# Kernel optimization log

Hardware: AMD Instinct MI355X
Metric: run time of the kernel (lower is better)

Reference implementation:

```python
import jax, jax.numpy as jnp
import numpy as np

D_MODEL = 1024
NUM_HEADS = 16
D_K = D_MODEL // NUM_HEADS
ROPE_THETA = 10000.0


def apply_rope(x, pos):
    # x: [B, H, S, d_k], pos: [S] int
    half = x.shape[-1] // 2
    inv_freq = ROPE_THETA ** (-jnp.arange(half, dtype=jnp.float32) * 2.0 / x.shape[-1])
    ang = pos.astype(jnp.float32)[:, None] * inv_freq[None, :]  # [S, half]
    cos, sin = jnp.cos(ang), jnp.sin(ang)
    x1 = x[..., 0::2]
    x2 = x[..., 1::2]
    r1 = x1 * cos - x2 * sin
    r2 = x1 * sin + x2 * cos
    return jnp.stack([r1, r2], axis=-1).reshape(x.shape)


def setup_inputs() -> dict:
    key = jax.random.key(0)
    ks = jax.random.split(key, 5)
    B, S = 4, 2048
    scale = 1.0 / np.sqrt(D_MODEL)
    x = jax.random.normal(ks[0], (B, S, D_MODEL), dtype=jnp.float32)
    w_q = jax.random.normal(ks[1], (D_MODEL, D_MODEL), dtype=jnp.float32) * scale
    w_k = jax.random.normal(ks[2], (D_MODEL, D_MODEL), dtype=jnp.float32) * scale
    w_v = jax.random.normal(ks[3], (D_MODEL, D_MODEL), dtype=jnp.float32) * scale
    w_o = jax.random.normal(ks[4], (D_MODEL, D_MODEL), dtype=jnp.float32) * scale
    token_positions = jnp.arange(S, dtype=jnp.int32)
    return {"x": x, "w_q": w_q, "w_k": w_k, "w_v": w_v, "w_o": w_o, "token_positions": token_positions}


def reference(x, w_q, w_k, w_v, w_o, token_positions):
    B, S, _ = x.shape
    def proj(w):
        return (x @ w.T).reshape(B, S, NUM_HEADS, D_K).transpose(0, 2, 1, 3)  # [B,H,S,d_k]
    q, k, v = proj(w_q), proj(w_k), proj(w_v)
    q = apply_rope(q, token_positions)
    k = apply_rope(k, token_positions)
    logits = jnp.einsum('bhid,bhjd->bhij', q, k) / jnp.sqrt(jnp.float32(D_K))
    causal = jnp.tril(jnp.ones((S, S), dtype=bool))
    logits = jnp.where(causal[None, None], logits, -jnp.inf)
    weights = jax.nn.softmax(logits, axis=-1)
    attn = jnp.einsum('bhij,bhjd->bhid', weights, v)  # [B,H,S,d_k]
    attn = attn.transpose(0, 2, 1, 3).reshape(B, S, D_MODEL)
    return attn @ w_o.T
```

## Files before the change

### kernel.cpp

```cpp
#include <hip/hip_runtime.h>
#include <hip/hip_bf16.h>
#include <stdint.h>

#define DM   1024
#define SEQ  2048
#define BATCH 4
#define NH   16
#define DK   64
#define NTK  16

typedef __attribute__((ext_vector_type(8))) __bf16 bf16x8;
typedef __attribute__((ext_vector_type(4))) float f32x4;
typedef __attribute__((ext_vector_type(4))) unsigned short ushort4_t;

typedef __attribute__((address_space(1))) const unsigned int GU32;
typedef __attribute__((address_space(3))) unsigned int LU32;

__device__ inline void gl_lds16(const void* g, void* l) {
  __builtin_amdgcn_global_load_lds((GU32*)g, (LU32*)l, 16, 0, 0);
}

__device__ inline f32x4 mfma16(bf16x8 a, bf16x8 b, f32x4 c) {
  return __builtin_amdgcn_mfma_f32_16x16x32_bf16(a, b, c, 0, 0, 0);
}

__device__ inline unsigned short f2bf(float f) {
  unsigned u = __float_as_uint(f);
  u += 0x7fffu + ((u >> 16) & 1u);
  return (unsigned short)(u >> 16);
}

__device__ inline unsigned cvt_pk_bf16(float a, float b) {
  unsigned r;
  asm("v_cvt_pk_bf16_f32 %0, %1, %2" : "=v"(r) : "v"(a), "v"(b));
  return r;
}

__device__ inline float fexp2(float x) {
  float r;
  asm("v_exp_f32 %0, %1" : "=v"(r) : "v"(x));
  return r;
}

__device__ inline int swz_of(int r) { return ((r & 6) << 2) | ((r & 1) << 5); }
__device__ inline int bswz(int r) { return ((r & 6) << 3) | ((r & 1) << 6); }

__global__ void prep_kernel(const float* __restrict__ x,
                            const float* __restrict__ wq, const float* __restrict__ wk,
                            const float* __restrict__ wv, const float* __restrict__ wo,
                            const int* __restrict__ tp,
                            unsigned short* __restrict__ xbf,
                            unsigned short* __restrict__ wbf,
                            float2* __restrict__ tab)
{
  const int NX4 = (BATCH*SEQ*DM)/4;
  const int NW4 = (DM*DM)/4;
  int idx = blockIdx.x*256 + threadIdx.x;
  if (idx < NX4) {
    float4 v = ((const float4*)x)[idx];
    ushort4_t o; o[0]=f2bf(v.x); o[1]=f2bf(v.y); o[2]=f2bf(v.z); o[3]=f2bf(v.w);
    ((ushort4_t*)xbf)[idx] = o;
  } else if (idx < NX4 + 4*NW4) {
    int t = idx - NX4;
    int wsel = t >> 18;
    int off = t & (NW4-1);
    const float* src = (wsel==0) ? wq : (wsel==1) ? wk : (wsel==2) ? wv : wo;
    float4 v = ((const float4*)src)[off];
    ushort4_t o; o[0]=f2bf(v.x); o[1]=f2bf(v.y); o[2]=f2bf(v.z); o[3]=f2bf(v.w);
    ((ushort4_t*)wbf)[wsel*NW4 + off] = o;
  } else {
    int t = idx - NX4 - 4*NW4;
    if (t < SEQ*32) {
      int s = t >> 5, i = t & 31;
      float invf = exp2f(-(float)i * (13.287712379549449f/32.0f));
      float ang = (float)tp[s] * invf;
      float sn, cs; sincosf(ang, &sn, &cs);
      tab[t] = make_float2(cs, sn);
    }
  }
}

template<int MODE>
__global__ __launch_bounds__(256, 2)
void gemm_db(const unsigned short* __restrict__ A,
             const unsigned short* __restrict__ Wall,
             unsigned short* __restrict__ qbf,
             unsigned short* __restrict__ kbf,
             unsigned short* __restrict__ vt,
             float* __restrict__ ofp,
             const float2* __restrict__ tab)
{
  __shared__ __align__(16) char lds[65536];
  const int tid = threadIdx.x;
  const int bid = blockIdx.x;
  int sel, mt, nt;
  if (MODE == 0) {
    sel = bid >> 9;
    int r = bid & 511;
    int xcd = r & 7, idx = r >> 3;
    mt = xcd*8 + (idx >> 3);  nt = idx & 7;
  } else {
    sel = 3;
    int xcd = bid & 7, idx = bid >> 3;
    mt = xcd*8 + (idx >> 3);  nt = idx & 7;
  }
  const unsigned short* Bm = Wall + (size_t)sel*DM*DM;
  const int a0 = mt*128, b0r = nt*128;
  const int w = tid>>6, lane = tid&63, ln = lane&15, g = lane>>4;
  const int wm = (w>>1)*64, wn = (w&1)*64;

  const char* src[8];
  {
    int rr = tid >> 3;
    int c  = (tid & 7) * 8;
    #pragma unroll
    for (int i = 0; i < 4; ++i) {
      int r_ = i*32 + rr;
      int cs = c ^ swz_of(r_);
      src[i]   = (const char*)(A  + (size_t)(a0  + r_)*DM + cs);
      src[i+4] = (const char*)(Bm + (size_t)(b0r + r_)*DM + cs);
    }
  }

  int offA[4], offB[4];
  #pragma unroll
  for (int m = 0; m < 4; ++m) {
    int R  = wm + m*16 + ln;
    offA[m] = R*128 + ((g*8 ^ swz_of(R)) * 2);
    int Rb = wn + m*16 + ln;
    offB[m] = 16384 + Rb*128 + ((g*8 ^ swz_of(Rb)) * 2);
  }

  f32x4 acc[4][4];
  #pragma unroll
  for (int i=0;i<4;i++)
    #pragma unroll
    for (int j=0;j<4;j++) acc[i][j] = (f32x4){0.f,0.f,0.f,0.f};

  #pragma unroll
  for (int i = 0; i < 8; ++i) gl_lds16(src[i],       lds +         i*4096 + tid*16);
  #pragma unroll
  for (int i = 0; i < 8; ++i) gl_lds16(src[i] + 128, lds + 32768 + i*4096 + tid*16);

  for (int t = 0; t < NTK; ++t) {
    char* sb = lds + (t & 1) * 32768;
    if (t < NTK-1) asm volatile("s_waitcnt vmcnt(8)" ::: "memory");
    else           asm volatile("s_waitcnt vmcnt(0)" ::: "memory");
    __builtin_amdgcn_sched_barrier(0);
    __builtin_amdgcn_s_barrier();
    asm volatile("" ::: "memory");
    __builtin_amdgcn_sched_barrier(0);

    bf16x8 fa[4][2], fb[4][2];
    #pragma unroll
    for (int m = 0; m < 4; ++m) {
      fa[m][0] = *(const bf16x8*)(sb + offA[m]);
      fa[m][1] = *(const bf16x8*)(sb + (offA[m] ^ 64));
      fb[m][0] = *(const bf16x8*)(sb + offB[m]);
      fb[m][1] = *(const bf16x8*)(sb + (offB[m] ^ 64));
    }
    asm volatile("s_waitcnt lgkmcnt(0)" ::: "memory");
    __builtin_amdgcn_sched_barrier(0);
    __builtin_amdgcn_s_barrier();
    asm volatile("" ::: "memory");
    __builtin_amdgcn_sched_barrier(0);

    if (t + 2 < NTK) {
      const int kb = (t + 2) * 128;
      #pragma unroll
      for (int i = 0; i < 8; ++i)
        gl_lds16(src[i] + kb, sb + i*4096 + tid*16);
    }
    __builtin_amdgcn_s_setprio(1);
    #pragma unroll
    for (int h = 0; h < 2; ++h)
      #pragma unroll
      for (int m = 0; m < 4; ++m)
        #pragma unroll
        for (int n = 0; n < 4; ++n)
          acc[m][n] = mfma16(fa[m][h], fb[n][h], acc[m][n]);
    __builtin_amdgcn_s_setprio(0);
  }

  if (MODE == 1) {
    #pragma unroll
    for (int i=0;i<4;i++) {
      int m = a0 + wm + i*16 + g*4;
      #pragma unroll
      for (int jn=0;jn<4;jn++) {
        int n = b0r + wn + jn*16 + ln;
        #pragma unroll
        for (int j=0;j<4;j++)
          ofp[(size_t)(m+j)*DM + n] = acc[i][jn][j];
      }
    }
  } else if (sel == 2) {
    #pragma unroll
    for (int i=0;i<4;i++) {
      int m0 = a0 + wm + i*16 + g*4;
      int bb = m0>>11, s0 = m0&2047;
      #pragma unroll
      for (int jn=0;jn<4;jn++) {
        int n = b0r + wn + jn*16 + ln;
        int h = n>>6, d = n&63;
        ushort4_t o4;
        #pragma unroll
        for (int j=0;j<4;j++) o4[j] = f2bf(acc[i][jn][j]);
        *(ushort4_t*)&vt[(((size_t)bb*NH + h)*DK + d)*SEQ + s0] = o4;
      }
    }
  } else {
    unsigned short* dst = sel ? kbf : qbf;
    const float qs = sel ? 1.0f : 0.1803368802f;
    #pragma unroll
    for (int jn=0;jn<4;jn++) {
      int n = b0r + wn + jn*16 + ln;
      int h = n>>6, d = n&63, di = d>>1, par = d&1;
      #pragma unroll
      for (int i=0;i<4;i++) {
        #pragma unroll
        for (int j=0;j<4;j++) {
          int m = a0 + wm + i*16 + g*4 + j;
          int bb = m>>11, s = m&2047;
          float v = acc[i][jn][j];
          float pv = __shfl_xor(v, 1);
          float2 cssn = tab[s*32 + di];
          float r = par ? (v*cssn.x + pv*cssn.y) : (v*cssn.x - pv*cssn.y);
          dst[((size_t)(bb*NH + h)*SEQ + s)*DK + d] = f2bf(r*qs);
        }
      }
    }
  }
}

__global__ __launch_bounds__(256, 2)
void attn_fa(const unsigned short* __restrict__ qbf,
             const unsigned short* __restrict__ kbf,
             const unsigned short* __restrict__ vtg,
             unsigned short* __restrict__ attnbf)
{
  __shared__ __align__(16) char kv_lds[32768];
  __shared__ unsigned short Pl[4][16][72];
  const int bh = blockIdx.x, qb = 31 - blockIdx.y;
  const int tid = threadIdx.x, w = tid>>6, lane = tid&63, ln = lane&15, g = lane>>4;
  const int q0 = qb*64 + w*16;

  const unsigned short* qrow = qbf + ((size_t)bh*SEQ + q0 + ln)*DK;
  bf16x8 qf0 = *(const bf16x8*)(qrow + g*8);
  bf16x8 qf1 = *(const bf16x8*)(qrow + 32 + g*8);

  const int rr = tid >> 3;
  const int cb = (tid & 7) * 16;
  const char* ks0 = (const char*)(kbf + ((size_t)bh*SEQ + rr     )*DK) + (cb ^ bswz(rr));
  const char* ks1 = (const char*)(kbf + ((size_t)bh*SEQ + rr + 32)*DK) + (cb ^ bswz(rr));
  const char* vs0 = (const char*)(vtg + ((size_t)bh*DK  + rr     )*SEQ) + (cb ^ bswz(rr));
  const char* vs1 = (const char*)(vtg + ((size_t)bh*DK  + rr + 32)*SEQ) + (cb ^ bswz(rr));

  const int ok0 = (g*16) ^ bswz(ln);

  {
    gl_lds16(ks0, kv_lds +         tid*16);
    gl_lds16(ks1, kv_lds +  4096 + tid*16);
    gl_lds16(vs0, kv_lds +  8192 + tid*16);
    gl_lds16(vs1, kv_lds + 12288 + tid*16);
    if (qb > 0) {
      gl_lds16(ks0 + 8192, kv_lds + 16384 +         tid*16);
      gl_lds16(ks1 + 8192, kv_lds + 16384 +  4096 + tid*16);
      gl_lds16(vs0 + 128,  kv_lds + 16384 +  8192 + tid*16);
      gl_lds16(vs1 + 128,  kv_lds + 16384 + 12288 + tid*16);
    }
  }

  f32x4 o[4];
  #pragma unroll
  for (int f=0;f<4;f++) o[f] = (f32x4){0.f,0.f,0.f,0.f};
  float m_run = -1e30f, l_run = 0.f;
  const int qg = q0 + ln;

  for (int t = 0; t <= qb; ++t) {
    char* sb = kv_lds + (t & 1) * 16384;
    if (t < qb) asm volatile("s_waitcnt vmcnt(4)" ::: "memory");
    else        asm volatile("s_waitcnt vmcnt(0)" ::: "memory");
    __builtin_amdgcn_sched_barrier(0);
    __builtin_amdgcn_s_barrier();
    asm volatile("" ::: "memory");
    __builtin_amdgcn_sched_barrier(0);

    bf16x8 kf[4][2], vfr[4][2];
    #pragma unroll
    for (int a=0;a<4;a++) {
      kf[a][0]  = *(const bf16x8*)(sb + a*2048 + (ok0 ^  0) + ln*128);
      kf[a][1]  = *(const bf16x8*)(sb + a*2048 + (ok0 ^ 64) + ln*128);
      vfr[a][0] = *(const bf16x8*)(sb + 8192 + a*2048 + (ok0 ^  0) + ln*128);
      vfr[a][1] = *(const bf16x8*)(sb + 8192 + a*2048 + (ok0 ^ 64) + ln*128);
    }
    asm volatile("s_waitcnt lgkmcnt(0)" ::: "memory");
    __builtin_amdgcn_sched_barrier(0);
    __builtin_amdgcn_s_barrier();
    asm volatile("" ::: "memory");
    __builtin_amdgcn_sched_barrier(0);

    if (t + 2 <= qb) {
      const size_t kO = (size_t)(t+2)*8192, vO = (size_t)(t+2)*128;
      gl_lds16(ks0 + kO, sb +         tid*16);
      gl_lds16(ks1 + kO, sb +  4096 + tid*16);
      gl_lds16(vs0 + vO, sb +  8192 + tid*16);
      gl_lds16(vs1 + vO, sb + 12288 + tid*16);
    }

    f32x4 sa[4];
    __builtin_amdgcn_s_setprio(1);
    #pragma unroll
    for (int kvf=0;kvf<4;kvf++) {
      f32x4 z = (f32x4){0.f,0.f,0.f,0.f};
      z = mfma16(kf[kvf][0], qf0, z);
      z = mfma16(kf[kvf][1], qf1, z);
      sa[kvf] = z;
    }
    __builtin_amdgcn_s_setprio(0);

    float lmax = -1e30f;
    if (t == qb) {
      const int kv0 = t*64;
      #pragma unroll
      for (int kvf=0;kvf<4;kvf++)
        #pragma unroll
        for (int j=0;j<4;j++) {
          int kv = kv0 + kvf*16 + g*4 + j;
          float v = (kv <= qg) ? sa[kvf][j] : -1e30f;
          sa[kvf][j] = v; lmax = fmaxf(lmax, v);
        }
    } else {
      #pragma unroll
      for (int kvf=0;kvf<4;kvf++)
        #pragma unroll
        for (int j=0;j<4;j++) lmax = fmaxf(lmax, sa[kvf][j]);
    }
    lmax = fmaxf(lmax, __shfl_xor(lmax, 16));
    lmax = fmaxf(lmax, __shfl_xor(lmax, 32));

    if (!__all(lmax - m_run <= 8.0f)) {
      float mnew = fmaxf(m_run, lmax);
      float corr = fexp2(m_run - mnew);
      l_run *= corr;
      #pragma unroll
      for (int j=0;j<4;j++) {
        float cj = __shfl(corr, g*4 + j);
        #pragma unroll
        for (int f=0;f<4;f++) o[f][j] *= cj;
      }
      m_run = mnew;
    }

    float lsum = 0.f;
    #pragma unroll
    for (int kvf=0;kvf<4;kvf++) {
      float p0 = fexp2(sa[kvf][0] - m_run);
      float p1 = fexp2(sa[kvf][1] - m_run);
      float p2 = fexp2(sa[kvf][2] - m_run);
      float p3 = fexp2(sa[kvf][3] - m_run);
      lsum += (p0+p1)+(p2+p3);
      uint2 pk;
      pk.x = cvt_pk_bf16(p0, p1);
      pk.y = cvt_pk_bf16(p2, p3);
      *(uint2*)&Pl[w][ln][kvf*16 + g*4] = pk;
    }
    lsum += __shfl_xor(lsum, 16);
    lsum += __shfl_xor(lsum, 32);
    l_run += lsum;

    asm volatile("s_waitcnt lgkmcnt(0)" ::: "memory");

    __builtin_amdgcn_s_setprio(1);
    #pragma unroll
    for (int c=0;c<2;c++) {
      bf16x8 pf = *(const bf16x8*)&Pl[w][ln][c*32 + g*8];
      #pragma unroll
      for (int f=0;f<4;f++)
        o[f] = mfma16(pf, vfr[f][c], o[f]);
    }
    __builtin_amdgcn_s_setprio(0);
  }

  const int bb = bh>>4, h = bh&15;
  #pragma unroll
  for (int j=0;j<4;j++) {
    float linv = 1.0f / __shfl(l_run, g*4 + j);
    int s = q0 + g*4 + j;
    #pragma unroll
    for (int f=0;f<4;f++)
      attnbf[((size_t)bb*SEQ + s)*DM + h*DK + f*16 + ln] = f2bf(o[f][j]*linv);
  }
}

extern "C" void kernel_launch(void* const* d_in, const int* in_sizes, int n_in,
                              void* d_out, int out_size, void* d_ws, size_t ws_size,
                              hipStream_t stream)
{
  const float* x  = (const float*)d_in[0];
  const float* wq = (const float*)d_in[1];
  const float* wk = (const float*)d_in[2];
  const float* wv = (const float*)d_in[3];
  const float* wo = (const float*)d_in[4];
  const int*   tp = (const int*)d_in[5];

  const size_t XB = (size_t)BATCH*SEQ*DM*2;
  const size_t WB = (size_t)DM*DM*2;

  char* ws = (char*)d_ws;
  unsigned short* xbf = (unsigned short*)(ws);
  unsigned short* qbf = (unsigned short*)(ws + XB);
  unsigned short* kbf = (unsigned short*)(ws + 2*XB);
  unsigned short* vt  = (unsigned short*)(ws + 3*XB);
  unsigned short* abf = (unsigned short*)(ws + 4*XB);
  unsigned short* wbf = (unsigned short*)(ws + 5*XB);
  float2* tab = (float2*)(ws + 5*XB + 4*WB);

  prep_kernel<<<12544, 256, 0, stream>>>(x, wq, wk, wv, wo, tp, xbf, wbf, tab);

  gemm_db<0><<<1536, 256, 0, stream>>>(xbf, wbf, qbf, kbf, vt, nullptr, tab);
  attn_fa<<<dim3(64,32), 256, 0, stream>>>(qbf, kbf, vt, abf);
  gemm_db<1><<<512, 256, 0, stream>>>(abf, wbf, nullptr, nullptr, nullptr,
                                      (float*)d_out, nullptr);
}
```

Before: 180.7 us.

## Process two query tiles per attention block to reuse each K/V tile

```diff
diff --git a/kernel.cpp b/kernel.cpp
--- a/kernel.cpp
+++ b/kernel.cpp
@@ -12,6 +12,7 @@
 typedef __attribute__((ext_vector_type(8))) __bf16 bf16x8;
 typedef __attribute__((ext_vector_type(4))) float f32x4;
 typedef __attribute__((ext_vector_type(4))) unsigned short ushort4_t;
+typedef __attribute__((ext_vector_type(4))) unsigned int uint4_t;
 
 typedef __attribute__((address_space(1))) const unsigned int GU32;
 typedef __attribute__((address_space(3))) unsigned int LU32;
@@ -39,6 +40,12 @@
 __device__ inline float fexp2(float x) {
   float r;
   asm("v_exp_f32 %0, %1" : "=v"(r) : "v"(x));
+  return r;
+}
+
+__device__ inline float fmax3(float a, float b, float c) {
+  float r;
+  asm("v_max3_f32 %0, %1, %2, %3" : "=v"(r) : "v"(a), "v"(b), "v"(c));
   return r;
 }
 
@@ -240,14 +247,23 @@
              unsigned short* __restrict__ attnbf)
 {
   __shared__ __align__(16) char kv_lds[32768];
-  __shared__ unsigned short Pl[4][16][72];
-  const int bh = blockIdx.x, qb = 31 - blockIdx.y;
+  __shared__ unsigned short PlA[4][16][72];
+  __shared__ unsigned short PlB[4][16][72];
+  const int bh = blockIdx.x, qblk = 15 - blockIdx.y;
   const int tid = threadIdx.x, w = tid>>6, lane = tid&63, ln = lane&15, g = lane>>4;
-  const int q0 = qb*64 + w*16;
-
-  const unsigned short* qrow = qbf + ((size_t)bh*SEQ + q0 + ln)*DK;
-  bf16x8 qf0 = *(const bf16x8*)(qrow + g*8);
-  bf16x8 qf1 = *(const bf16x8*)(qrow + 32 + g*8);
+  const int q0a = qblk*128 + w*16;
+  const int q0b = q0a + 64;
+  const int NT = 2*qblk + 2;
+
+  const unsigned short* qrowA = qbf + ((size_t)bh*SEQ + q0a + ln)*DK;
+  const unsigned short* qrowB = qbf + ((size_t)bh*SEQ + q0b + ln)*DK;
+  bf16x8 qa0 = *(const bf16x8*)(qrowA + g*8);
+  bf16x8 qa1 = *(const bf16x8*)(qrowA + 32 + g*8);
+  bf16x8 qb0 = *(const bf16x8*)(qrowB + g*8);
+  bf16x8 qb1 = *(const bf16x8*)(qrowB + 32 + g*8);
+
+  uint4_t ov = {0x3F803F80u, 0x3F803F80u, 0x3F803F80u, 0x3F803F80u};
+  const bf16x8 ones = *(bf16x8*)&ov;
 
   const int rr = tid >> 3;
   const int cb = (tid & 7) * 16;
@@ -258,29 +274,26 @@
 
   const int ok0 = (g*16) ^ bswz(ln);
 
-  {
-    gl_lds16(ks0, kv_lds +         tid*16);
-    gl_lds16(ks1, kv_lds +  4096 + tid*16);
-    gl_lds16(vs0, kv_lds +  8192 + tid*16);
-    gl_lds16(vs1, kv_lds + 12288 + tid*16);
-    if (qb > 0) {
-      gl_lds16(ks0 + 8192, kv_lds + 16384 +         tid*16);
-      gl_lds16(ks1 + 8192, kv_lds + 16384 +  4096 + tid*16);
-      gl_lds16(vs0 + 128,  kv_lds + 16384 +  8192 + tid*16);
-      gl_lds16(vs1 + 128,  kv_lds + 16384 + 12288 + tid*16);
-    }
-  }
-
-  f32x4 o[4];
+  gl_lds16(ks0, kv_lds +         tid*16);
+  gl_lds16(ks1, kv_lds +  4096 + tid*16);
+  gl_lds16(vs0, kv_lds +  8192 + tid*16);
+  gl_lds16(vs1, kv_lds + 12288 + tid*16);
+  gl_lds16(ks0 + 8192, kv_lds + 16384 +         tid*16);
+  gl_lds16(ks1 + 8192, kv_lds + 16384 +  4096 + tid*16);
+  gl_lds16(vs0 + 128,  kv_lds + 16384 +  8192 + tid*16);
+  gl_lds16(vs1 + 128,  kv_lds + 16384 + 12288 + tid*16);
+
+  f32x4 oA[4], oB[4], osA, osB;
   #pragma unroll
-  for (int f=0;f<4;f++) o[f] = (f32x4){0.f,0.f,0.f,0.f};
-  float m_run = -1e30f, l_run = 0.f;
-  const int qg = q0 + ln;
-
-  for (int t = 0; t <= qb; ++t) {
+  for (int f=0;f<4;f++) { oA[f] = (f32x4){0,0,0,0}; oB[f] = (f32x4){0,0,0,0}; }
+  osA = (f32x4){0,0,0,0}; osB = (f32x4){0,0,0,0};
+  float mA = -1e30f, mB = -1e30f;
+  const int qgA = q0a + ln, qgB = q0b + ln;
+
+  for (int t = 0; t < NT; ++t) {
     char* sb = kv_lds + (t & 1) * 16384;
-    if (t < qb) asm volatile("s_waitcnt vmcnt(4)" ::: "memory");
-    else        asm volatile("s_waitcnt vmcnt(0)" ::: "memory");
+    if (t < NT-1) asm volatile("s_waitcnt vmcnt(4)" ::: "memory");
+    else          asm volatile("s_waitcnt vmcnt(0)" ::: "memory");
     __builtin_amdgcn_sched_barrier(0);
     __builtin_amdgcn_s_barrier();
     asm volatile("" ::: "memory");
@@ -300,7 +313,7 @@
     asm volatile("" ::: "memory");
     __builtin_amdgcn_sched_barrier(0);
 
-    if (t + 2 <= qb) {
+    if (t + 2 < NT) {
       const size_t kO = (size_t)(t+2)*8192, vO = (size_t)(t+2)*128;
       gl_lds16(ks0 + kO, sb +         tid*16);
       gl_lds16(ks1 + kO, sb +  4096 + tid*16);
@@ -308,76 +321,136 @@
       gl_lds16(vs1 + vO, sb + 12288 + tid*16);
     }
 
-    f32x4 sa[4];
+    const bool actA = (t < NT-1);
+
+    f32x4 saA[4], saB[4];
     __builtin_amdgcn_s_setprio(1);
     #pragma unroll
     for (int kvf=0;kvf<4;kvf++) {
-      f32x4 z = (f32x4){0.f,0.f,0.f,0.f};
-      z = mfma16(kf[kvf][0], qf0, z);
-      z = mfma16(kf[kvf][1], qf1, z);
-      sa[kvf] = z;
+      f32x4 zb = (f32x4){0,0,0,0};
+      zb = mfma16(kf[kvf][0], qb0, zb);
+      zb = mfma16(kf[kvf][1], qb1, zb);
+      saB[kvf] = zb;
+    }
+    if (actA) {
+      #pragma unroll
+      for (int kvf=0;kvf<4;kvf++) {
+        f32x4 za = (f32x4){0,0,0,0};
+        za = mfma16(kf[kvf][0], qa0, za);
+        za = mfma16(kf[kvf][1], qa1, za);
+        saA[kvf] = za;
+      }
     }
     __builtin_amdgcn_s_setprio(0);
 
-    float lmax = -1e30f;
-    if (t == qb) {
-      const int kv0 = t*64;
-      #pragma unroll
-      for (int kvf=0;kvf<4;kvf++)
+    if (actA) {
+      if (t == NT-2) {
+        int thr = qgA - t*64 - g*4;
+        #pragma unroll
+        for (int kvf=0;kvf<4;kvf++)
+          #pragma unroll
+          for (int j=0;j<4;j++)
+            if (kvf*16 + j > thr) saA[kvf][j] = -1e30f;
+      }
+      float lm = fmax3(saA[0][0], saA[0][1], saA[0][2]);
+      lm = fmax3(lm, saA[0][3], saA[1][0]);
+      lm = fmax3(lm, saA[1][1], saA[1][2]);
+      lm = fmax3(lm, saA[1][3], saA[2][0]);
+      lm = fmax3(lm, saA[2][1], saA[2][2]);
+      lm = fmax3(lm, saA[2][3], saA[3][0]);
+      lm = fmax3(lm, saA[3][1], saA[3][2]);
+      lm = fmaxf(lm, saA[3][3]);
+      lm = fmaxf(lm, __shfl_xor(lm, 16));
+      lm = fmaxf(lm, __shfl_xor(lm, 32));
+      if (!__all(lm - mA <= 8.0f)) {
+        float mnew = fmaxf(mA, lm);
+        float corr = fexp2(mA - mnew);
         #pragma unroll
         for (int j=0;j<4;j++) {
-          int kv = kv0 + kvf*16 + g*4 + j;
-          float v = (kv <= qg) ? sa[kvf][j] : -1e30f;
-          sa[kvf][j] = v; lmax = fmaxf(lmax, v);
+          float cj = __shfl(corr, g*4 + j);
+          #pragma unroll
+          for (int f=0;f<4;f++) oA[f][j] *= cj;
+          osA[j] *= cj;
         }
-    } else {
-      #pragma unroll
-      for (int kvf=0;kvf<4;kvf++)
-        #pragma unroll
-        for (int j=0;j<4;j++) lmax = fmaxf(lmax, sa[kvf][j]);
-    }
-    lmax = fmaxf(lmax, __shfl_xor(lmax, 16));
-    lmax = fmaxf(lmax, __shfl_xor(lmax, 32));
-
-    if (!__all(lmax - m_run <= 8.0f)) {
-      float mnew = fmaxf(m_run, lmax);
-      float corr = fexp2(m_run - mnew);
-      l_run *= corr;
-      #pragma unroll
-      for (int j=0;j<4;j++) {
-        float cj = __shfl(corr, g*4 + j);
-        #pragma unroll
-        for (int f=0;f<4;f++) o[f][j] *= cj;
-      }
-      m_run = mnew;
-    }
-
-    float lsum = 0.f;
-    #pragma unroll
-    for (int kvf=0;kvf<4;kvf++) {
-      float p0 = fexp2(sa[kvf][0] - m_run);
-      float p1 = fexp2(sa[kvf][1] - m_run);
-      float p2 = fexp2(sa[kvf][2] - m_run);
-      float p3 = fexp2(sa[kvf][3] - m_run);
-      lsum += (p0+p1)+(p2+p3);
-      uint2 pk;
-      pk.x = cvt_pk_bf16(p0, p1);
-      pk.y = cvt_pk_bf16(p2, p3);
-      *(uint2*)&Pl[w][ln][kvf*16 + g*4] = pk;
-    }
-    lsum += __shfl_xor(lsum, 16);
-    lsum += __shfl_xor(lsum, 32);
-    l_run += lsum;
+        mA = mnew;
+      }
+      #pragma unroll
+      for (int kvf=0;kvf<4;kvf++) {
+        float p0 = fexp2(saA[kvf][0] - mA);
+        float p1 = fexp2(saA[kvf][1] - mA);
+        float p2 = fexp2(saA[kvf][2] - mA);
+        float p3 = fexp2(saA[kvf][3] - mA);
+        uint2 pk;
+        pk.x = cvt_pk_bf16(p0, p1);
+        pk.y = cvt_pk_bf16(p2, p3);
+        *(uint2*)&PlA[w][ln][kvf*16 + g*4] = pk;
+      }
+    }
+
+    {
+      if (t == NT-1) {
+        int thr = qgB - t*64 - g*4;
+        #pragma unroll
+        for (int kvf=0;kvf<4;kvf++)
+          #pragma unroll
+          for (int j=0;j<4;j++)
+            if (kvf*16 + j > thr) saB[kvf][j] = -1e30f;
+      }
+      float lm = fmax3(saB[0][0], saB[0][1], saB[0][2]);
+      lm = fmax3(lm, saB[0][3], saB[1][0]);
+      lm = fmax3(lm, saB[1][1], saB[1][2]);
+      lm = fmax3(lm, saB[1][3], saB[2][0]);
+      lm = fmax3(lm, saB[2][1], saB[2][2]);
+      lm = fmax3(lm, saB[2][3], saB[3][0]);
+      lm = fmax3(lm, saB[3][1], saB[3][2]);
+      lm = fmaxf(lm, saB[3][3]);
+      lm = fmaxf(lm, __shfl_xor(lm, 16));
+      lm = fmaxf(lm, __shfl_xor(lm, 32));
+      if (!__all(lm - mB <= 8.0f)) {
+        float mnew = fmaxf(mB, lm);
+        float corr = fexp2(mB - mnew);
+        #pragma unroll
+        for (int j=0;j<4;j++) {
+          float cj = __shfl(corr, g*4 + j);
+          #pragma unroll
+          for (int f=0;f<4;f++) oB[f][j] *= cj;
+          osB[j] *= cj;
+        }
+        mB = mnew;
+      }
+      #pragma unroll
+      for (int kvf=0;kvf<4;kvf++) {
+        float p0 = fexp2(saB[kvf][0] - mB);
+        float p1 = fexp2(saB[kvf][1] - mB);
+        float p2 = fexp2(saB[kvf][2] - mB);
+        float p3 = fexp2(saB[kvf][3] - mB);
+        uint2 pk;
+        pk.x = cvt_pk_bf16(p0, p1);
+        pk.y = cvt_pk_bf16(p2, p3);
+        *(uint2*)&PlB[w][ln][kvf*16 + g*4] = pk;
+      }
+    }
 
     asm volatile("s_waitcnt lgkmcnt(0)" ::: "memory");
 
     __builtin_amdgcn_s_setprio(1);
     #pragma unroll
     for (int c=0;c<2;c++) {
-      bf16x8 pf = *(const bf16x8*)&Pl[w][ln][c*32 + g*8];
+      bf16x8 pfB = *(const bf16x8*)&PlB[w][ln][c*32 + g*8];
       #pragma unroll
       for (int f=0;f<4;f++)
-        o[f] = mfma16(pf, vfr[f][c], o[f]);
+        oB[f] = mfma16(pfB, vfr[f][c], oB[f]);
+      osB = mfma16(pfB, ones, osB);
+    }
+    if (actA) {
+      #pragma unroll
+      for (int c=0;c<2;c++) {
+        bf16x8 pfA = *(const bf16x8*)&PlA[w][ln][c*32 + g*8];
+        #pragma unroll
+        for (int f=0;f<4;f++)
+          oA[f] = mfma16(pfA, vfr[f][c], oA[f]);
+        osA = mfma16(pfA, ones, osA);
+      }
     }
     __builtin_amdgcn_s_setprio(0);
   }
@@ -385,11 +458,14 @@
   const int bb = bh>>4, h = bh&15;
   #pragma unroll
   for (int j=0;j<4;j++) {
-    float linv = 1.0f / __shfl(l_run, g*4 + j);
-    int s = q0 + g*4 + j;
-    #pragma unroll
-    for (int f=0;f<4;f++)
-      attnbf[((size_t)bb*SEQ + s)*DM + h*DK + f*16 + ln] = f2bf(o[f][j]*linv);
+    float liA = 1.0f / osA[j];
+    float liB = 1.0f / osB[j];
+    int sA = q0a + g*4 + j, sB = q0b + g*4 + j;
+    #pragma unroll
+    for (int f=0;f<4;f++) {
+      attnbf[((size_t)bb*SEQ + sA)*DM + h*DK + f*16 + ln] = f2bf(oA[f][j]*liA);
+      attnbf[((size_t)bb*SEQ + sB)*DM + h*DK + f*16 + ln] = f2bf(oB[f][j]*liB);
+    }
   }
 }
 
@@ -419,7 +495,7 @@
   prep_kernel<<<12544, 256, 0, stream>>>(x, wq, wk, wv, wo, tp, xbf, wbf, tab);
 
   gemm_db<0><<<1536, 256, 0, stream>>>(xbf, wbf, qbf, kbf, vt, nullptr, tab);
-  attn_fa<<<dim3(64,32), 256, 0, stream>>>(qbf, kbf, vt, abf);
+  attn_fa<<<dim3(64,16), 256, 0, stream>>>(qbf, kbf, vt, abf);
   gemm_db<1><<<512, 256, 0, stream>>>(abf, wbf, nullptr, nullptr, nullptr,
                                       (float*)d_out, nullptr);
 }
```

Result: faster. 176.0 us (-2.6%).

## Pair causal query blocks per workgroup and compute row sums via MFMA

Applied to the files above, without the earlier changes.

```diff
diff --git a/kernel.cpp b/kernel.cpp
--- a/kernel.cpp
+++ b/kernel.cpp
@@ -12,6 +12,7 @@
 typedef __attribute__((ext_vector_type(8))) __bf16 bf16x8;
 typedef __attribute__((ext_vector_type(4))) float f32x4;
 typedef __attribute__((ext_vector_type(4))) unsigned short ushort4_t;
+typedef __attribute__((ext_vector_type(4))) unsigned int uint4_t;
 
 typedef __attribute__((address_space(1))) const unsigned int GU32;
 typedef __attribute__((address_space(3))) unsigned int LU32;
@@ -39,6 +40,12 @@
 __device__ inline float fexp2(float x) {
   float r;
   asm("v_exp_f32 %0, %1" : "=v"(r) : "v"(x));
+  return r;
+}
+
+__device__ inline float fmax3(float a, float b, float c) {
+  float r;
+  asm("v_max3_f32 %0, %1, %2, %3" : "=v"(r) : "v"(a), "v"(b), "v"(c));
   return r;
 }
 
@@ -240,14 +247,16 @@
              unsigned short* __restrict__ attnbf)
 {
   __shared__ __align__(16) char kv_lds[32768];
-  __shared__ unsigned short Pl[4][16][72];
-  const int bh = blockIdx.x, qb = 31 - blockIdx.y;
+  __shared__ __align__(16) char pl_lds[8192];
+  const int bh = blockIdx.x, pr = blockIdx.y;
+  const int qbA = 31 - pr;
+  const int NTa = qbA + 1;
+  const int NTtot = 33;
   const int tid = threadIdx.x, w = tid>>6, lane = tid&63, ln = lane&15, g = lane>>4;
-  const int q0 = qb*64 + w*16;
-
-  const unsigned short* qrow = qbf + ((size_t)bh*SEQ + q0 + ln)*DK;
-  bf16x8 qf0 = *(const bf16x8*)(qrow + g*8);
-  bf16x8 qf1 = *(const bf16x8*)(qrow + 32 + g*8);
+  const int bb = bh>>4, h = bh&15;
+
+  uint4_t ov = {0x3F803F80u, 0x3F803F80u, 0x3F803F80u, 0x3F803F80u};
+  const bf16x8 ones = *(bf16x8*)&ov;
 
   const int rr = tid >> 3;
   const int cb = (tid & 7) * 16;
@@ -257,30 +266,35 @@
   const char* vs1 = (const char*)(vtg + ((size_t)bh*DK  + rr + 32)*SEQ) + (cb ^ bswz(rr));
 
   const int ok0 = (g*16) ^ bswz(ln);
-
-  {
-    gl_lds16(ks0, kv_lds +         tid*16);
-    gl_lds16(ks1, kv_lds +  4096 + tid*16);
-    gl_lds16(vs0, kv_lds +  8192 + tid*16);
-    gl_lds16(vs1, kv_lds + 12288 + tid*16);
-    if (qb > 0) {
-      gl_lds16(ks0 + 8192, kv_lds + 16384 +         tid*16);
-      gl_lds16(ks1 + 8192, kv_lds + 16384 +  4096 + tid*16);
-      gl_lds16(vs0 + 128,  kv_lds + 16384 +  8192 + tid*16);
-      gl_lds16(vs1 + 128,  kv_lds + 16384 + 12288 + tid*16);
-    }
-  }
-
-  f32x4 o[4];
-  #pragma unroll
-  for (int f=0;f<4;f++) o[f] = (f32x4){0.f,0.f,0.f,0.f};
-  float m_run = -1e30f, l_run = 0.f;
-  const int qg = q0 + ln;
-
-  for (int t = 0; t <= qb; ++t) {
-    char* sb = kv_lds + (t & 1) * 16384;
-    if (t < qb) asm volatile("s_waitcnt vmcnt(4)" ::: "memory");
-    else        asm volatile("s_waitcnt vmcnt(0)" ::: "memory");
+  char* plw = pl_lds + w*2048 + ln*128;
+  const int plswz = (ln & 7) << 4;
+
+  gl_lds16(ks0, kv_lds +         tid*16);
+  gl_lds16(ks1, kv_lds +  4096 + tid*16);
+  gl_lds16(vs0, kv_lds +  8192 + tid*16);
+  gl_lds16(vs1, kv_lds + 12288 + tid*16);
+  gl_lds16(ks0 + 8192, kv_lds + 16384 +         tid*16);
+  gl_lds16(ks1 + 8192, kv_lds + 16384 +  4096 + tid*16);
+  gl_lds16(vs0 + 128,  kv_lds + 16384 +  8192 + tid*16);
+  gl_lds16(vs1 + 128,  kv_lds + 16384 + 12288 + tid*16);
+
+  int q0 = qbA*64 + w*16;
+  const unsigned short* qrow = qbf + ((size_t)bh*SEQ + q0 + ln)*DK;
+  bf16x8 qf0 = *(const bf16x8*)(qrow + g*8);
+  bf16x8 qf1 = *(const bf16x8*)(qrow + 32 + g*8);
+
+  f32x4 o[4], os;
+  #pragma unroll
+  for (int f=0;f<4;f++) o[f] = (f32x4){0,0,0,0};
+  os = (f32x4){0,0,0,0};
+  float m_run = -1e30f;
+
+  for (int u = 0; u < NTtot; ++u) {
+    const int tloc  = (u < NTa) ? u : u - NTa;
+    const int NTcur = (u < NTa) ? NTa : NTtot - NTa;
+    char* sb = kv_lds + (u & 1) * 16384;
+    if (u < NTtot-1) asm volatile("s_waitcnt vmcnt(4)" ::: "memory");
+    else             asm volatile("s_waitcnt vmcnt(0)" ::: "memory");
     __builtin_amdgcn_sched_barrier(0);
     __builtin_amdgcn_s_barrier();
     asm volatile("" ::: "memory");
@@ -300,96 +314,108 @@
     asm volatile("" ::: "memory");
     __builtin_amdgcn_sched_barrier(0);
 
-    if (t + 2 <= qb) {
-      const size_t kO = (size_t)(t+2)*8192, vO = (size_t)(t+2)*128;
+    if (u + 2 < NTtot) {
+      const int t2 = (u + 2 < NTa) ? u + 2 : u + 2 - NTa;
+      const size_t kO = (size_t)t2*8192, vO = (size_t)t2*128;
       gl_lds16(ks0 + kO, sb +         tid*16);
       gl_lds16(ks1 + kO, sb +  4096 + tid*16);
       gl_lds16(vs0 + vO, sb +  8192 + tid*16);
       gl_lds16(vs1 + vO, sb + 12288 + tid*16);
     }
 
+    if (u == NTa) {
+      #pragma unroll
+      for (int j=0;j<4;j++) {
+        float li = 1.0f / os[j];
+        int s = q0 + g*4 + j;
+        #pragma unroll
+        for (int f=0;f<4;f++)
+          attnbf[((size_t)bb*SEQ + s)*DM + h*DK + f*16 + ln] = f2bf(o[f][j]*li);
+      }
+      q0 = pr*64 + w*16;
+      const unsigned short* qr = qbf + ((size_t)bh*SEQ + q0 + ln)*DK;
+      qf0 = *(const bf16x8*)(qr + g*8);
+      qf1 = *(const bf16x8*)(qr + 32 + g*8);
+      #pragma unroll
+      for (int f=0;f<4;f++) o[f] = (f32x4){0,0,0,0};
+      os = (f32x4){0,0,0,0};
+      m_run = -1e30f;
+    }
+
     f32x4 sa[4];
     __builtin_amdgcn_s_setprio(1);
     #pragma unroll
     for (int kvf=0;kvf<4;kvf++) {
-      f32x4 z = (f32x4){0.f,0.f,0.f,0.f};
+      f32x4 z = (f32x4){0,0,0,0};
       z = mfma16(kf[kvf][0], qf0, z);
       z = mfma16(kf[kvf][1], qf1, z);
       sa[kvf] = z;
     }
     __builtin_amdgcn_s_setprio(0);
 
-    float lmax = -1e30f;
-    if (t == qb) {
-      const int kv0 = t*64;
+    if (tloc == NTcur-1) {
+      int thr = q0 + ln - tloc*64 - g*4;
       #pragma unroll
       for (int kvf=0;kvf<4;kvf++)
         #pragma unroll
-        for (int j=0;j<4;j++) {
-          int kv = kv0 + kvf*16 + g*4 + j;
-          float v = (kv <= qg) ? sa[kvf][j] : -1e30f;
-          sa[kvf][j] = v; lmax = fmaxf(lmax, v);
-        }
-    } else {
-      #pragma unroll
-      for (int kvf=0;kvf<4;kvf++)
-        #pragma unroll
-        for (int j=0;j<4;j++) lmax = fmaxf(lmax, sa[kvf][j]);
-    }
-    lmax = fmaxf(lmax, __shfl_xor(lmax, 16));
-    lmax = fmaxf(lmax, __shfl_xor(lmax, 32));
-
-    if (!__all(lmax - m_run <= 8.0f)) {
-      float mnew = fmaxf(m_run, lmax);
+        for (int j=0;j<4;j++)
+          if (kvf*16 + j > thr) sa[kvf][j] = -1e30f;
+    }
+    float lm = fmax3(sa[0][0], sa[0][1], sa[0][2]);
+    lm = fmax3(lm, sa[0][3], sa[1][0]);
+    lm = fmax3(lm, sa[1][1], sa[1][2]);
+    lm = fmax3(lm, sa[1][3], sa[2][0]);
+    lm = fmax3(lm, sa[2][1], sa[2][2]);
+    lm = fmax3(lm, sa[2][3], sa[3][0]);
+    lm = fmax3(lm, sa[3][1], sa[3][2]);
+    lm = fmaxf(lm, sa[3][3]);
+    lm = fmaxf(lm, __shfl_xor(lm, 16));
+    lm = fmaxf(lm, __shfl_xor(lm, 32));
+    if (!__all(lm - m_run <= 8.0f)) {
+      float mnew = fmaxf(m_run, lm);
       float corr = fexp2(m_run - mnew);
-      l_run *= corr;
       #pragma unroll
       for (int j=0;j<4;j++) {
         float cj = __shfl(corr, g*4 + j);
         #pragma unroll
         for (int f=0;f<4;f++) o[f][j] *= cj;
+        os[j] *= cj;
       }
       m_run = mnew;
     }
-
-    float lsum = 0.f;
     #pragma unroll
     for (int kvf=0;kvf<4;kvf++) {
       float p0 = fexp2(sa[kvf][0] - m_run);
       float p1 = fexp2(sa[kvf][1] - m_run);
       float p2 = fexp2(sa[kvf][2] - m_run);
       float p3 = fexp2(sa[kvf][3] - m_run);
-      lsum += (p0+p1)+(p2+p3);
       uint2 pk;
       pk.x = cvt_pk_bf16(p0, p1);
       pk.y = cvt_pk_bf16(p2, p3);
-      *(uint2*)&Pl[w][ln][kvf*16 + g*4] = pk;
-    }
-    lsum += __shfl_xor(lsum, 16);
-    lsum += __shfl_xor(lsum, 32);
-    l_run += lsum;
-
+      *(uint2*)(plw + ((kvf*32 + g*8) ^ plswz)) = pk;
+    }
     asm volatile("s_waitcnt lgkmcnt(0)" ::: "memory");
+    __builtin_amdgcn_sched_barrier(0);
 
     __builtin_amdgcn_s_setprio(1);
     #pragma unroll
     for (int c=0;c<2;c++) {
-      bf16x8 pf = *(const bf16x8*)&Pl[w][ln][c*32 + g*8];
+      bf16x8 pf = *(const bf16x8*)(plw + ((c*64 + g*16) ^ plswz));
       #pragma unroll
       for (int f=0;f<4;f++)
         o[f] = mfma16(pf, vfr[f][c], o[f]);
+      os = mfma16(pf, ones, os);
     }
     __builtin_amdgcn_s_setprio(0);
   }
 
-  const int bb = bh>>4, h = bh&15;
   #pragma unroll
   for (int j=0;j<4;j++) {
-    float linv = 1.0f / __shfl(l_run, g*4 + j);
+    float li = 1.0f / os[j];
     int s = q0 + g*4 + j;
     #pragma unroll
     for (int f=0;f<4;f++)
-      attnbf[((size_t)bb*SEQ + s)*DM + h*DK + f*16 + ln] = f2bf(o[f][j]*linv);
+      attnbf[((size_t)bb*SEQ + s)*DM + h*DK + f*16 + ln] = f2bf(o[f][j]*li);
   }
 }
 
@@ -419,7 +445,7 @@
   prep_kernel<<<12544, 256, 0, stream>>>(x, wq, wk, wv, wo, tp, xbf, wbf, tab);
 
   gemm_db<0><<<1536, 256, 0, stream>>>(xbf, wbf, qbf, kbf, vt, nullptr, tab);
-  attn_fa<<<dim3(64,32), 256, 0, stream>>>(qbf, kbf, vt, abf);
+  attn_fa<<<dim3(64,16), 256, 0, stream>>>(qbf, kbf, vt, abf);
   gemm_db<1><<<512, 256, 0, stream>>>(abf, wbf, nullptr, nullptr, nullptr,
                                       (float*)d_out, nullptr);
 }
```

New measurement: 177.4 us. Within noise of the previous version (-1.8%).
